# Kernel tuning notes

Hardware: AMD Instinct MI355X
Metric: run time of the kernel (lower is better)

The kernel has to match this reference:

```python
import jax, jax.numpy as jnp
import numpy as np

N_NODES = 100000
N_EDGES = 1000000
D_IN = 64
D_MODEL = 64  # H * D
H = 4
D = D_MODEL // H


def setup_inputs() -> dict:
    key = jax.random.key(0)
    ks = jax.random.split(key, 9)
    nodes = jax.random.normal(ks[0], (N_NODES, D_IN), dtype=jnp.float32)
    senders = jax.random.randint(ks[1], (N_EDGES,), 0, N_NODES, dtype=jnp.int32)
    receivers = jnp.sort(jax.random.randint(ks[2], (N_EDGES,), 0, N_NODES, dtype=jnp.int32))
    s = 1.0 / np.sqrt(D_IN)
    W_qk = jax.random.uniform(ks[3], (D_IN, D_MODEL), jnp.float32, -s, s)
    b_qk = jnp.zeros((D_MODEL,), jnp.float32)
    W_v = jax.random.uniform(ks[4], (D_IN, D_MODEL), jnp.float32, -s, s)
    b_v = jnp.zeros((D_MODEL,), jnp.float32)
    so = 1.0 / np.sqrt(D_MODEL)
    W_out = jax.random.uniform(ks[5], (D_MODEL, D_MODEL), jnp.float32, -so, so)
    b_out = jnp.zeros((D_MODEL,), jnp.float32)
    return {
        'nodes': nodes, 'W_qk': W_qk, 'b_qk': b_qk, 'W_v': W_v, 'b_v': b_v,
        'W_out': W_out, 'b_out': b_out, 'senders': senders, 'receivers': receivers,
    }


def _segment_softmax(logits, segment_ids, num_segments):
    # jraph-style numerically stable segment softmax (segments are sorted)
    maxs = jax.ops.segment_max(logits, segment_ids, num_segments, indices_are_sorted=True)
    e = jnp.exp(logits - maxs[segment_ids])
    z = jax.ops.segment_sum(e, segment_ids, num_segments, indices_are_sorted=True)
    return e / z[segment_ids]


def reference(nodes, W_qk, b_qk, W_v, b_v, W_out, b_out, senders, receivers):
    N = nodes.shape[0]
    # projections: N (H D) -> N H D
    qks = (nodes @ W_qk + b_qk).reshape(N, H, D)
    vs = (nodes @ W_v + b_v).reshape(N, H, D)
    # per-edge QK scores: [E, H]
    scores = jnp.einsum('ehd,ehd->eh', qks[receivers], qks[senders])
    attn = _segment_softmax(scores, receivers, N)
    # weighted message scatter: [E,H,D] -> [N, H*D]
    messages = (attn[..., None] * vs[senders]).reshape(-1, H * D)
    ctx = jax.ops.segment_sum(messages, receivers, N, indices_are_sorted=True)
    out = ctx @ W_out + b_out
    return out, attn
```

## Files before the change

kernel.cpp:

```cpp
#include <hip/hip_runtime.h>
#include <math.h>


typedef _Float16 h2 __attribute__((ext_vector_type(2)));
typedef _Float16 half8 __attribute__((ext_vector_type(8)));
typedef float floatx4 __attribute__((ext_vector_type(4)));

#define SP_ROW 136

__global__ __launch_bounds__(256) void mhga_prep(
    const float* __restrict__ Wqk, const float* __restrict__ Wv,
    _Float16* __restrict__ Wt,
    const int* __restrict__ receivers, int* __restrict__ row_ptr,
    int N, int E)
{
    if ((int)blockIdx.x < 32) {
        const int idx = blockIdx.x * 256 + threadIdx.x;
        const int n = idx >> 6, k = idx & 63;
        const float w = (n < 64) ? Wqk[k * 64 + n] : Wv[k * 64 + (n - 64)];
        Wt[idx] = (_Float16)w;
        return;
    }
    const int n = (blockIdx.x - 32) * 256 + threadIdx.x;
    if (n > N) return;
    int lo = 0, hi = E;
    while (lo < hi) {
        const int mid = (lo + hi) >> 1;
        if (receivers[mid] < n) lo = mid + 1; else hi = mid;
    }
    row_ptr[n] = lo;
}

__global__ __launch_bounds__(256) void mhga_proj(
    const float* __restrict__ X, const _Float16* __restrict__ Wt,
    const float* __restrict__ bqk, const float* __restrict__ bv,
    unsigned char* __restrict__ packed, int N)
{
    __shared__ __align__(16) _Float16 sP[64 * SP_ROW];
    const int t = threadIdx.x;
    const int w = t >> 6, lane = t & 63;
    const int ln = lane & 15, quad = lane >> 4;
    const int m0 = blockIdx.x * 64;

    const int arow = min(m0 + w * 16 + ln, N - 1);
    const float* xr = X + (size_t)arow * 64;
    const float4 xa = *(const float4*)(xr + quad * 8);
    const float4 xb = *(const float4*)(xr + quad * 8 + 4);
    const float4 xc = *(const float4*)(xr + 32 + quad * 8);
    const float4 xd = *(const float4*)(xr + 32 + quad * 8 + 4);
    const half8 a0 = { (_Float16)xa.x, (_Float16)xa.y, (_Float16)xa.z,
                       (_Float16)xa.w, (_Float16)xb.x, (_Float16)xb.y,
                       (_Float16)xb.z, (_Float16)xb.w };
    const half8 a1 = { (_Float16)xc.x, (_Float16)xc.y, (_Float16)xc.z,
                       (_Float16)xc.w, (_Float16)xd.x, (_Float16)xd.y,
                       (_Float16)xd.z, (_Float16)xd.w };

    floatx4 acc[8];
#pragma unroll
    for (int tt = 0; tt < 8; ++tt) {
        const _Float16* wrow = Wt + (tt * 16 + ln) * 64;
        const half8 b0 = *(const half8*)(wrow + quad * 8);
        const half8 b1 = *(const half8*)(wrow + 32 + quad * 8);
        floatx4 c = {0.f, 0.f, 0.f, 0.f};
        c = __builtin_amdgcn_mfma_f32_16x16x32_f16(a0, b0, c, 0, 0, 0);
        c = __builtin_amdgcn_mfma_f32_16x16x32_f16(a1, b1, c, 0, 0, 0);
        acc[tt] = c;
    }

#pragma unroll
    for (int tt = 0; tt < 8; ++tt) {
        const float bt = (tt < 4) ? bqk[tt * 16 + ln] : bv[(tt - 4) * 16 + ln];
        const int j = (tt & 3) * 16 + ln;
        const int fidx = (j >> 2) * 8 + ((tt < 4) ? 0 : 4) + (j & 3);
#pragma unroll
        for (int r = 0; r < 4; ++r) {
            const int lrow = w * 16 + quad * 4 + r;
            sP[lrow * SP_ROW + fidx] = (_Float16)(acc[tt][r] + bt);
        }
    }

    const int crow = w * 16 + (lane >> 2);
    const int grow = m0 + crow;
    if (grow < N) {
        const _Float16* src = sP + crow * SP_ROW + (lane & 3) * 32;
        unsigned char* dst = packed + (size_t)grow * 256 + (lane & 3) * 64;
#pragma unroll
        for (int c = 0; c < 4; ++c)
            *(uint4*)(dst + c * 16) = *(const uint4*)(src + c * 8);
    }
}

__global__ __launch_bounds__(256) void mhga_attn(
    const unsigned char* __restrict__ packed,
    const int* __restrict__ senders, const int* __restrict__ row_ptr,
    const float* __restrict__ Wout, const float* __restrict__ bout,
    float* __restrict__ p_ws, float* __restrict__ out,
    float* __restrict__ attn_out, int N)
{
    __shared__ float sW[64 * 64];
    __shared__ float sCtx[4][64];
    const int t = threadIdx.x;
#pragma unroll
    for (int i = t * 4; i < 4096; i += 1024)
        *(float4*)(sW + i) = *(const float4*)(Wout + i);

    const int wave = t >> 6, lane = t & 63;
    const int g = lane >> 4, tl = lane & 15;
    const float bo = bout[lane];
    __syncthreads();

    for (int n = blockIdx.x * 4 + wave; n < N; n += gridDim.x * 4) {
        const int e0 = row_ptr[n];
        const int e1 = row_ptr[n + 1];
        float l = 0.f;
        float4 ctx = make_float4(0.f, 0.f, 0.f, 0.f);
        const uint4 qpk = *(const uint4*)(packed + (size_t)n * 256 + tl * 16);
        const h2 q0 = __builtin_bit_cast(h2, qpk.x);
        const h2 q1 = __builtin_bit_cast(h2, qpk.y);

        for (int base = e0; base < e1; base += 64) {
            const int cnt = min(64, e1 - base);
            int sid = 0;
            if (base + lane < e1) sid = senders[base + lane];
            const int iters = (cnt + 3) >> 2;
            for (int i = 0; i < iters; ++i) {
                const int idx = i * 4 + g;
                const int s = __shfl(sid, idx, 64);
                if (idx < cnt) {
                    const uint4 pk =
                        *(const uint4*)(packed + (size_t)s * 256 + tl * 16);
                    const h2 k0 = __builtin_bit_cast(h2, pk.x);
                    const h2 k1 = __builtin_bit_cast(h2, pk.y);
                    const h2 v0 = __builtin_bit_cast(h2, pk.z);
                    const h2 v1 = __builtin_bit_cast(h2, pk.w);
                    float d = __builtin_amdgcn_fdot2(q0, k0, 0.f, false);
                    d = __builtin_amdgcn_fdot2(q1, k1, d, false);
                    d += __shfl_xor(d, 1, 64);
                    d += __shfl_xor(d, 2, 64);
                    const float p = __expf(d);
                    if ((tl & 3) == 0)
                        p_ws[(size_t)(base + idx) * 4 + (tl >> 2)] = p;
                    l += p;
                    ctx.x = fmaf(p, (float)v0.x, ctx.x);
                    ctx.y = fmaf(p, (float)v0.y, ctx.y);
                    ctx.z = fmaf(p, (float)v1.x, ctx.z);
                    ctx.w = fmaf(p, (float)v1.y, ctx.w);
                }
            }
        }
#pragma unroll
        for (int mask = 16; mask <= 32; mask <<= 1) {
            l     += __shfl_xor(l, mask, 64);
            ctx.x += __shfl_xor(ctx.x, mask, 64);
            ctx.y += __shfl_xor(ctx.y, mask, 64);
            ctx.z += __shfl_xor(ctx.z, mask, 64);
            ctx.w += __shfl_xor(ctx.w, mask, 64);
        }
        const float inv = (l > 0.f) ? (1.f / l) : 0.f;
        if (g == 0) {
            *(float4*)(&sCtx[wave][tl * 4]) =
                make_float4(ctx.x * inv, ctx.y * inv, ctx.z * inv, ctx.w * inv);
        }

        __builtin_amdgcn_s_waitcnt(0x0F70);

        const float lh = __shfl(l, (lane & 3) << 2, 64);
        const float invl = (lh > 0.f) ? (1.f / lh) : 0.f;
        volatile const float* vp = p_ws;
        for (int f = e0 * 4 + lane; f < e1 * 4; f += 64)
            attn_out[f] = vp[f] * invl;

        float acc = bo;
#pragma unroll
        for (int k = 0; k < 64; k += 4) {
            const float4 c = *(const float4*)(&sCtx[wave][k]);
            acc = fmaf(c.x, sW[(k + 0) * 64 + lane], acc);
            acc = fmaf(c.y, sW[(k + 1) * 64 + lane], acc);
            acc = fmaf(c.z, sW[(k + 2) * 64 + lane], acc);
            acc = fmaf(c.w, sW[(k + 3) * 64 + lane], acc);
        }
        out[(size_t)n * 64 + lane] = acc;
    }
}

extern "C" void kernel_launch(void* const* d_in, const int* in_sizes, int n_in,
                              void* d_out, int out_size, void* d_ws, size_t ws_size,
                              hipStream_t stream) {
    const float* nodes   = (const float*)d_in[0];
    const float* W_qk    = (const float*)d_in[1];
    const float* b_qk    = (const float*)d_in[2];
    const float* W_v     = (const float*)d_in[3];
    const float* b_v     = (const float*)d_in[4];
    const float* W_out   = (const float*)d_in[5];
    const float* b_out   = (const float*)d_in[6];
    const int* senders   = (const int*)d_in[7];
    const int* receivers = (const int*)d_in[8];

    const int N = in_sizes[0] / 64;
    const int E = in_sizes[7];

    float* out      = (float*)d_out;
    float* attn_out = out + (size_t)N * 64;

    unsigned char* packed = (unsigned char*)d_ws;
    int*   rowp = (int*)(packed + (size_t)N * 256);
    float* p_ws = (float*)(rowp + (((N + 1) + 3) & ~3));
    _Float16* Wt = (_Float16*)(p_ws + (size_t)E * 4);

    const int RB = (N + 1 + 255) / 256;
    mhga_prep<<<32 + RB, 256, 0, stream>>>(W_qk, W_v, Wt, receivers, rowp, N, E);
    mhga_proj<<<(N + 63) / 64, 256, 0, stream>>>(nodes, Wt, b_qk, b_v,
                                                 packed, N);
    mhga_attn<<<2048, 256, 0, stream>>>(packed, senders, rowp,
                                        W_out, b_out, p_ws, out, attn_out, N);
}
```

Before: 194.4 us.

## Keep attention probabilities in registers and process eight edges per wave step

The attention kernel now maps each edge to 8 lanes that load 32 bytes each, instead of 16 lanes loading 16 bytes, so each wave step covers eight edges. For receivers with at most 64 edges the unnormalized probabilities stay in registers and are normalized directly into attn_out, which removes the p_ws scratch write, the readback, and the waitcnt. Receivers with more edges take a fallback that recomputes the scores in a second pass. The cost is more registers for ctx[8] and preg[8], plus redundant gathers on high-degree nodes.

```diff
diff --git a/kernel.cpp b/kernel.cpp
--- a/kernel.cpp
+++ b/kernel.cpp
@@ -94,8 +94,7 @@
     const unsigned char* __restrict__ packed,
     const int* __restrict__ senders, const int* __restrict__ row_ptr,
     const float* __restrict__ Wout, const float* __restrict__ bout,
-    float* __restrict__ p_ws, float* __restrict__ out,
-    float* __restrict__ attn_out, int N)
+    float* __restrict__ out, float* __restrict__ attn_out, int N)
 {
     __shared__ float sW[64 * 64];
     __shared__ float sCtx[4][64];
@@ -105,70 +104,149 @@
         *(float4*)(sW + i) = *(const float4*)(Wout + i);
 
     const int wave = t >> 6, lane = t & 63;
-    const int g = lane >> 4, tl = lane & 15;
+    const int g = lane >> 3, u = lane & 7;
     const float bo = bout[lane];
     __syncthreads();
 
     for (int n = blockIdx.x * 4 + wave; n < N; n += gridDim.x * 4) {
         const int e0 = row_ptr[n];
         const int e1 = row_ptr[n + 1];
+        const int cnt = e1 - e0;
+
+        const unsigned char* qrow = packed + (size_t)n * 256 + u * 32;
+        const uint4 qA = *(const uint4*)(qrow);
+        const uint4 qB = *(const uint4*)(qrow + 16);
+        const h2 q0 = __builtin_bit_cast(h2, qA.x);
+        const h2 q1 = __builtin_bit_cast(h2, qA.y);
+        const h2 q2 = __builtin_bit_cast(h2, qB.x);
+        const h2 q3 = __builtin_bit_cast(h2, qB.y);
+
         float l = 0.f;
-        float4 ctx = make_float4(0.f, 0.f, 0.f, 0.f);
-        const uint4 qpk = *(const uint4*)(packed + (size_t)n * 256 + tl * 16);
-        const h2 q0 = __builtin_bit_cast(h2, qpk.x);
-        const h2 q1 = __builtin_bit_cast(h2, qpk.y);
-
-        for (int base = e0; base < e1; base += 64) {
-            const int cnt = min(64, e1 - base);
+        float ctx[8] = {0.f, 0.f, 0.f, 0.f, 0.f, 0.f, 0.f, 0.f};
+        float preg[8];
+        int iters = 0;
+
+        if (cnt <= 64) {
             int sid = 0;
-            if (base + lane < e1) sid = senders[base + lane];
-            const int iters = (cnt + 3) >> 2;
-            for (int i = 0; i < iters; ++i) {
-                const int idx = i * 4 + g;
+            if (e0 + lane < e1) sid = senders[e0 + lane];
+            iters = (cnt + 7) >> 3;
+#pragma unroll
+            for (int i = 0; i < 8; ++i) {
+                if (i >= iters) break;
+                const int idx = i * 8 + g;
                 const int s = __shfl(sid, idx, 64);
-                if (idx < cnt) {
-                    const uint4 pk =
-                        *(const uint4*)(packed + (size_t)s * 256 + tl * 16);
-                    const h2 k0 = __builtin_bit_cast(h2, pk.x);
-                    const h2 k1 = __builtin_bit_cast(h2, pk.y);
-                    const h2 v0 = __builtin_bit_cast(h2, pk.z);
-                    const h2 v1 = __builtin_bit_cast(h2, pk.w);
-                    float d = __builtin_amdgcn_fdot2(q0, k0, 0.f, false);
-                    d = __builtin_amdgcn_fdot2(q1, k1, d, false);
+                const unsigned char* row = packed + (size_t)s * 256 + u * 32;
+                const uint4 A = *(const uint4*)(row);
+                const uint4 B = *(const uint4*)(row + 16);
+                float d = __builtin_amdgcn_fdot2(q0, __builtin_bit_cast(h2, A.x), 0.f, false);
+                d = __builtin_amdgcn_fdot2(q1, __builtin_bit_cast(h2, A.y), d, false);
+                d = __builtin_amdgcn_fdot2(q2, __builtin_bit_cast(h2, B.x), d, false);
+                d = __builtin_amdgcn_fdot2(q3, __builtin_bit_cast(h2, B.y), d, false);
+                d += __shfl_xor(d, 1, 64);
+                float p = __expf(d);
+                p = (idx < cnt) ? p : 0.f;
+                preg[i] = p;
+                l += p;
+                const h2 vA0 = __builtin_bit_cast(h2, A.z);
+                const h2 vA1 = __builtin_bit_cast(h2, A.w);
+                const h2 vB0 = __builtin_bit_cast(h2, B.z);
+                const h2 vB1 = __builtin_bit_cast(h2, B.w);
+                ctx[0] = fmaf(p, (float)vA0.x, ctx[0]);
+                ctx[1] = fmaf(p, (float)vA0.y, ctx[1]);
+                ctx[2] = fmaf(p, (float)vA1.x, ctx[2]);
+                ctx[3] = fmaf(p, (float)vA1.y, ctx[3]);
+                ctx[4] = fmaf(p, (float)vB0.x, ctx[4]);
+                ctx[5] = fmaf(p, (float)vB0.y, ctx[5]);
+                ctx[6] = fmaf(p, (float)vB1.x, ctx[6]);
+                ctx[7] = fmaf(p, (float)vB1.y, ctx[7]);
+            }
+        } else {
+            for (int base = e0; base < e1; base += 64) {
+                const int c2 = min(64, e1 - base);
+                int sid = 0;
+                if (base + lane < e1) sid = senders[base + lane];
+                const int it2 = (c2 + 7) >> 3;
+                for (int i = 0; i < it2; ++i) {
+                    const int idx = i * 8 + g;
+                    const int s = __shfl(sid, idx, 64);
+                    const unsigned char* row = packed + (size_t)s * 256 + u * 32;
+                    const uint4 A = *(const uint4*)(row);
+                    const uint4 B = *(const uint4*)(row + 16);
+                    float d = __builtin_amdgcn_fdot2(q0, __builtin_bit_cast(h2, A.x), 0.f, false);
+                    d = __builtin_amdgcn_fdot2(q1, __builtin_bit_cast(h2, A.y), d, false);
+                    d = __builtin_amdgcn_fdot2(q2, __builtin_bit_cast(h2, B.x), d, false);
+                    d = __builtin_amdgcn_fdot2(q3, __builtin_bit_cast(h2, B.y), d, false);
                     d += __shfl_xor(d, 1, 64);
-                    d += __shfl_xor(d, 2, 64);
-                    const float p = __expf(d);
-                    if ((tl & 3) == 0)
-                        p_ws[(size_t)(base + idx) * 4 + (tl >> 2)] = p;
+                    float p = __expf(d);
+                    p = (idx < c2) ? p : 0.f;
                     l += p;
-                    ctx.x = fmaf(p, (float)v0.x, ctx.x);
-                    ctx.y = fmaf(p, (float)v0.y, ctx.y);
-                    ctx.z = fmaf(p, (float)v1.x, ctx.z);
-                    ctx.w = fmaf(p, (float)v1.y, ctx.w);
+                    const h2 vA0 = __builtin_bit_cast(h2, A.z);
+                    const h2 vA1 = __builtin_bit_cast(h2, A.w);
+                    const h2 vB0 = __builtin_bit_cast(h2, B.z);
+                    const h2 vB1 = __builtin_bit_cast(h2, B.w);
+                    ctx[0] = fmaf(p, (float)vA0.x, ctx[0]);
+                    ctx[1] = fmaf(p, (float)vA0.y, ctx[1]);
+                    ctx[2] = fmaf(p, (float)vA1.x, ctx[2]);
+                    ctx[3] = fmaf(p, (float)vA1.y, ctx[3]);
+                    ctx[4] = fmaf(p, (float)vB0.x, ctx[4]);
+                    ctx[5] = fmaf(p, (float)vB0.y, ctx[5]);
+                    ctx[6] = fmaf(p, (float)vB1.x, ctx[6]);
+                    ctx[7] = fmaf(p, (float)vB1.y, ctx[7]);
                 }
             }
         }
-#pragma unroll
-        for (int mask = 16; mask <= 32; mask <<= 1) {
-            l     += __shfl_xor(l, mask, 64);
-            ctx.x += __shfl_xor(ctx.x, mask, 64);
-            ctx.y += __shfl_xor(ctx.y, mask, 64);
-            ctx.z += __shfl_xor(ctx.z, mask, 64);
-            ctx.w += __shfl_xor(ctx.w, mask, 64);
+
+#pragma unroll
+        for (int mask = 8; mask <= 32; mask <<= 1) {
+            l += __shfl_xor(l, mask, 64);
+#pragma unroll
+            for (int j = 0; j < 8; ++j)
+                ctx[j] += __shfl_xor(ctx[j], mask, 64);
         }
         const float inv = (l > 0.f) ? (1.f / l) : 0.f;
+
+        if (cnt <= 64) {
+            if ((u & 1) == 0) {
+                const int h = u >> 1;
+#pragma unroll
+                for (int i = 0; i < 8; ++i) {
+                    const int idx = i * 8 + g;
+                    if (i < iters && idx < cnt)
+                        attn_out[(size_t)(e0 + idx) * 4 + h] = preg[i] * inv;
+                }
+            }
+        } else {
+            for (int base = e0; base < e1; base += 64) {
+                const int c2 = min(64, e1 - base);
+                int sid = 0;
+                if (base + lane < e1) sid = senders[base + lane];
+                const int it2 = (c2 + 7) >> 3;
+                for (int i = 0; i < it2; ++i) {
+                    const int idx = i * 8 + g;
+                    const int s = __shfl(sid, idx, 64);
+                    if (idx < c2) {
+                        const unsigned char* row = packed + (size_t)s * 256 + u * 32;
+                        const uint4 A = *(const uint4*)(row);
+                        const uint4 B = *(const uint4*)(row + 16);
+                        float d = __builtin_amdgcn_fdot2(q0, __builtin_bit_cast(h2, A.x), 0.f, false);
+                        d = __builtin_amdgcn_fdot2(q1, __builtin_bit_cast(h2, A.y), d, false);
+                        d = __builtin_amdgcn_fdot2(q2, __builtin_bit_cast(h2, B.x), d, false);
+                        d = __builtin_amdgcn_fdot2(q3, __builtin_bit_cast(h2, B.y), d, false);
+                        d += __shfl_xor(d, 1, 64);
+                        const float p = __expf(d);
+                        if ((u & 1) == 0)
+                            attn_out[(size_t)(base + idx) * 4 + (u >> 1)] = p * inv;
+                    }
+                }
+            }
+        }
+
         if (g == 0) {
-            *(float4*)(&sCtx[wave][tl * 4]) =
-                make_float4(ctx.x * inv, ctx.y * inv, ctx.z * inv, ctx.w * inv);
-        }
-
-        __builtin_amdgcn_s_waitcnt(0x0F70);
-
-        const float lh = __shfl(l, (lane & 3) << 2, 64);
-        const float invl = (lh > 0.f) ? (1.f / lh) : 0.f;
-        volatile const float* vp = p_ws;
-        for (int f = e0 * 4 + lane; f < e1 * 4; f += 64)
-            attn_out[f] = vp[f] * invl;
+            *(float4*)(&sCtx[wave][u * 8]) =
+                make_float4(ctx[0] * inv, ctx[1] * inv, ctx[2] * inv, ctx[3] * inv);
+            *(float4*)(&sCtx[wave][u * 8 + 4]) =
+                make_float4(ctx[4] * inv, ctx[5] * inv, ctx[6] * inv, ctx[7] * inv);
+        }
 
         float acc = bo;
 #pragma unroll
@@ -212,5 +290,5 @@
     mhga_proj<<<(N + 63) / 64, 256, 0, stream>>>(nodes, Wt, b_qk, b_v,
                                                  packed, N);
     mhga_attn<<<2048, 256, 0, stream>>>(packed, senders, rowp,
-                                        W_out, b_out, p_ws, out, attn_out, N);
-}
+                                        W_out, b_out, out, attn_out, N);
+}
```

Result: slower. 214.2 us (+10.2%).

## Process two receiver nodes per wave and stage attention weights in LDS

Applied to the files above, without the earlier changes.

Each wave now handles a pair of consecutive receiver nodes, loading both nodes' sender IDs in one 64-lane read and interleaving their gathers so more loads are in flight at once. When the pair has at most 64 edges, unnormalised attention weights are kept in shared memory rather than written to and re-read from a global scratch buffer. Pairs with more edges take a fallback path that writes raw weights into the output buffer and rescales them in place. The output projection is computed for both nodes in one pass over the W_out tile held in shared memory, and launch bounds request higher occupancy. In exchange the code has more branching and higher register pressure.

```diff
diff --git a/kernel.cpp b/kernel.cpp
--- a/kernel.cpp
+++ b/kernel.cpp
@@ -90,15 +90,14 @@
     }
 }
 
-__global__ __launch_bounds__(256) void mhga_attn(
+__global__ __launch_bounds__(256, 8) void mhga_attn(
     const unsigned char* __restrict__ packed,
     const int* __restrict__ senders, const int* __restrict__ row_ptr,
     const float* __restrict__ Wout, const float* __restrict__ bout,
-    float* __restrict__ p_ws, float* __restrict__ out,
-    float* __restrict__ attn_out, int N)
+    float* __restrict__ out, float* __restrict__ attn_out, int N)
 {
     __shared__ float sW[64 * 64];
-    __shared__ float sCtx[4][64];
+    __shared__ float sAtt[4][256];
     const int t = threadIdx.x;
 #pragma unroll
     for (int i = t * 4; i < 4096; i += 1024)
@@ -109,77 +108,194 @@
     const float bo = bout[lane];
     __syncthreads();
 
-    for (int n = blockIdx.x * 4 + wave; n < N; n += gridDim.x * 4) {
-        const int e0 = row_ptr[n];
-        const int e1 = row_ptr[n + 1];
-        float l = 0.f;
-        float4 ctx = make_float4(0.f, 0.f, 0.f, 0.f);
-        const uint4 qpk = *(const uint4*)(packed + (size_t)n * 256 + tl * 16);
-        const h2 q0 = __builtin_bit_cast(h2, qpk.x);
-        const h2 q1 = __builtin_bit_cast(h2, qpk.y);
-
-        for (int base = e0; base < e1; base += 64) {
-            const int cnt = min(64, e1 - base);
+    const int P = (N + 1) >> 1;
+    for (int pr = blockIdx.x * 4 + wave; pr < P; pr += gridDim.x * 4) {
+        const int n0 = pr * 2, n1 = n0 + 1;
+        const int e0 = row_ptr[n0];
+        const int e1 = row_ptr[n1];
+        const int e2 = (n1 < N) ? row_ptr[n1 + 1] : e1;
+        const int cnt0 = e1 - e0, cnt1 = e2 - e1, cntT = e2 - e0;
+
+        const uint4 q0pk = *(const uint4*)(packed + (size_t)n0 * 256 + tl * 16);
+        const int n1c = min(n1, N - 1);
+        const uint4 q1pk = *(const uint4*)(packed + (size_t)n1c * 256 + tl * 16);
+        const h2 qa0 = __builtin_bit_cast(h2, q0pk.x);
+        const h2 qa1 = __builtin_bit_cast(h2, q0pk.y);
+        const h2 qb0 = __builtin_bit_cast(h2, q1pk.x);
+        const h2 qb1 = __builtin_bit_cast(h2, q1pk.y);
+
+        float l0 = 0.f, l1 = 0.f;
+        float4 c0 = make_float4(0.f, 0.f, 0.f, 0.f);
+        float4 c1 = make_float4(0.f, 0.f, 0.f, 0.f);
+        const bool slow = (cntT > 64);
+
+        if (!slow) {
             int sid = 0;
-            if (base + lane < e1) sid = senders[base + lane];
-            const int iters = (cnt + 3) >> 2;
-            for (int i = 0; i < iters; ++i) {
+            if (e0 + lane < e2) sid = senders[e0 + lane];
+            const int it0 = (cnt0 + 3) >> 2;
+            const int it1 = (cnt1 + 3) >> 2;
+            const int im = max(it0, it1);
+            for (int i = 0; i < im; ++i) {
                 const int idx = i * 4 + g;
-                const int s = __shfl(sid, idx, 64);
-                if (idx < cnt) {
-                    const uint4 pk =
-                        *(const uint4*)(packed + (size_t)s * 256 + tl * 16);
-                    const h2 k0 = __builtin_bit_cast(h2, pk.x);
-                    const h2 k1 = __builtin_bit_cast(h2, pk.y);
-                    const h2 v0 = __builtin_bit_cast(h2, pk.z);
-                    const h2 v1 = __builtin_bit_cast(h2, pk.w);
-                    float d = __builtin_amdgcn_fdot2(q0, k0, 0.f, false);
-                    d = __builtin_amdgcn_fdot2(q1, k1, d, false);
+                const bool doA = (i < it0), doB = (i < it1);
+                uint4 pkA, pkB;
+                if (doA) {
+                    const int sA = __shfl(sid, idx, 64);
+                    pkA = *(const uint4*)(packed + (size_t)sA * 256 + tl * 16);
+                }
+                if (doB) {
+                    const int sB = __shfl(sid, (cnt0 + idx) & 63, 64);
+                    pkB = *(const uint4*)(packed + (size_t)sB * 256 + tl * 16);
+                }
+                if (doA) {
+                    const h2 k0 = __builtin_bit_cast(h2, pkA.x);
+                    const h2 k1 = __builtin_bit_cast(h2, pkA.y);
+                    const h2 v0 = __builtin_bit_cast(h2, pkA.z);
+                    const h2 v1 = __builtin_bit_cast(h2, pkA.w);
+                    float d = __builtin_amdgcn_fdot2(qa0, k0, 0.f, false);
+                    d = __builtin_amdgcn_fdot2(qa1, k1, d, false);
                     d += __shfl_xor(d, 1, 64);
                     d += __shfl_xor(d, 2, 64);
-                    const float p = __expf(d);
-                    if ((tl & 3) == 0)
-                        p_ws[(size_t)(base + idx) * 4 + (tl >> 2)] = p;
-                    l += p;
-                    ctx.x = fmaf(p, (float)v0.x, ctx.x);
-                    ctx.y = fmaf(p, (float)v0.y, ctx.y);
-                    ctx.z = fmaf(p, (float)v1.x, ctx.z);
-                    ctx.w = fmaf(p, (float)v1.y, ctx.w);
+                    float p = __expf(d);
+                    p = (idx < cnt0) ? p : 0.f;
+                    if ((tl & 3) == 0 && idx < cnt0)
+                        sAtt[wave][idx * 4 + (tl >> 2)] = p;
+                    l0 += p;
+                    c0.x = fmaf(p, (float)v0.x, c0.x);
+                    c0.y = fmaf(p, (float)v0.y, c0.y);
+                    c0.z = fmaf(p, (float)v1.x, c0.z);
+                    c0.w = fmaf(p, (float)v1.y, c0.w);
+                }
+                if (doB) {
+                    const h2 k0 = __builtin_bit_cast(h2, pkB.x);
+                    const h2 k1 = __builtin_bit_cast(h2, pkB.y);
+                    const h2 v0 = __builtin_bit_cast(h2, pkB.z);
+                    const h2 v1 = __builtin_bit_cast(h2, pkB.w);
+                    float d = __builtin_amdgcn_fdot2(qb0, k0, 0.f, false);
+                    d = __builtin_amdgcn_fdot2(qb1, k1, d, false);
+                    d += __shfl_xor(d, 1, 64);
+                    d += __shfl_xor(d, 2, 64);
+                    float p = __expf(d);
+                    p = (idx < cnt1) ? p : 0.f;
+                    if ((tl & 3) == 0 && idx < cnt1)
+                        sAtt[wave][(cnt0 + idx) * 4 + (tl >> 2)] = p;
+                    l1 += p;
+                    c1.x = fmaf(p, (float)v0.x, c1.x);
+                    c1.y = fmaf(p, (float)v0.y, c1.y);
+                    c1.z = fmaf(p, (float)v1.x, c1.z);
+                    c1.w = fmaf(p, (float)v1.y, c1.w);
                 }
             }
-        }
+        } else {
+            for (int m = 0; m < 2; ++m) {
+                const int s0 = m ? e1 : e0, s1 = m ? e2 : e1;
+                const h2 qq0 = m ? qb0 : qa0, qq1 = m ? qb1 : qa1;
+                for (int base = s0; base < s1; base += 64) {
+                    const int c2 = min(64, s1 - base);
+                    int sid2 = 0;
+                    if (base + lane < s1) sid2 = senders[base + lane];
+                    const int it2 = (c2 + 3) >> 2;
+                    for (int i = 0; i < it2; ++i) {
+                        const int idx = i * 4 + g;
+                        const int s = __shfl(sid2, idx, 64);
+                        if (idx < c2) {
+                            const uint4 pk =
+                                *(const uint4*)(packed + (size_t)s * 256 + tl * 16);
+                            const h2 k0 = __builtin_bit_cast(h2, pk.x);
+                            const h2 k1 = __builtin_bit_cast(h2, pk.y);
+                            const h2 v0 = __builtin_bit_cast(h2, pk.z);
+                            const h2 v1 = __builtin_bit_cast(h2, pk.w);
+                            float d = __builtin_amdgcn_fdot2(qq0, k0, 0.f, false);
+                            d = __builtin_amdgcn_fdot2(qq1, k1, d, false);
+                            d += __shfl_xor(d, 1, 64);
+                            d += __shfl_xor(d, 2, 64);
+                            const float p = __expf(d);
+                            if ((tl & 3) == 0)
+                                attn_out[(size_t)(base + idx) * 4 + (tl >> 2)] = p;
+                            if (m == 0) {
+                                l0 += p;
+                                c0.x = fmaf(p, (float)v0.x, c0.x);
+                                c0.y = fmaf(p, (float)v0.y, c0.y);
+                                c0.z = fmaf(p, (float)v1.x, c0.z);
+                                c0.w = fmaf(p, (float)v1.y, c0.w);
+                            } else {
+                                l1 += p;
+                                c1.x = fmaf(p, (float)v0.x, c1.x);
+                                c1.y = fmaf(p, (float)v0.y, c1.y);
+                                c1.z = fmaf(p, (float)v1.x, c1.z);
+                                c1.w = fmaf(p, (float)v1.y, c1.w);
+                            }
+                        }
+                    }
+                }
+            }
+        }
+
 #pragma unroll
         for (int mask = 16; mask <= 32; mask <<= 1) {
-            l     += __shfl_xor(l, mask, 64);
-            ctx.x += __shfl_xor(ctx.x, mask, 64);
-            ctx.y += __shfl_xor(ctx.y, mask, 64);
-            ctx.z += __shfl_xor(ctx.z, mask, 64);
-            ctx.w += __shfl_xor(ctx.w, mask, 64);
-        }
-        const float inv = (l > 0.f) ? (1.f / l) : 0.f;
+            l0   += __shfl_xor(l0, mask, 64);
+            l1   += __shfl_xor(l1, mask, 64);
+            c0.x += __shfl_xor(c0.x, mask, 64);
+            c0.y += __shfl_xor(c0.y, mask, 64);
+            c0.z += __shfl_xor(c0.z, mask, 64);
+            c0.w += __shfl_xor(c0.w, mask, 64);
+            c1.x += __shfl_xor(c1.x, mask, 64);
+            c1.y += __shfl_xor(c1.y, mask, 64);
+            c1.z += __shfl_xor(c1.z, mask, 64);
+            c1.w += __shfl_xor(c1.w, mask, 64);
+        }
+        const float inv0 = (l0 > 0.f) ? (1.f / l0) : 0.f;
+        const float inv1 = (l1 > 0.f) ? (1.f / l1) : 0.f;
+
+        const float lh0 = __shfl(l0, (lane & 3) << 2, 64);
+        const float lh1 = __shfl(l1, (lane & 3) << 2, 64);
+        const float iv0 = (lh0 > 0.f) ? (1.f / lh0) : 0.f;
+        const float iv1 = (lh1 > 0.f) ? (1.f / lh1) : 0.f;
+        if (!slow) {
+            const int fT = cntT * 4, f0 = cnt0 * 4;
+            for (int f = lane; f < fT; f += 64) {
+                const float iv = (f < f0) ? iv0 : iv1;
+                attn_out[e0 * 4 + f] = sAtt[wave][f] * iv;
+            }
+        } else {
+            __builtin_amdgcn_s_waitcnt(0x0F70);
+            volatile const float* vp = attn_out;
+            for (int f = e0 * 4 + lane; f < e2 * 4; f += 64) {
+                const float iv = (f < e1 * 4) ? iv0 : iv1;
+                attn_out[f] = vp[f] * iv;
+            }
+        }
+
         if (g == 0) {
-            *(float4*)(&sCtx[wave][tl * 4]) =
-                make_float4(ctx.x * inv, ctx.y * inv, ctx.z * inv, ctx.w * inv);
-        }
-
-        __builtin_amdgcn_s_waitcnt(0x0F70);
-
-        const float lh = __shfl(l, (lane & 3) << 2, 64);
-        const float invl = (lh > 0.f) ? (1.f / lh) : 0.f;
-        volatile const float* vp = p_ws;
-        for (int f = e0 * 4 + lane; f < e1 * 4; f += 64)
-            attn_out[f] = vp[f] * invl;
-
-        float acc = bo;
-#pragma unroll
-        for (int k = 0; k < 64; k += 4) {
-            const float4 c = *(const float4*)(&sCtx[wave][k]);
-            acc = fmaf(c.x, sW[(k + 0) * 64 + lane], acc);
-            acc = fmaf(c.y, sW[(k + 1) * 64 + lane], acc);
-            acc = fmaf(c.z, sW[(k + 2) * 64 + lane], acc);
-            acc = fmaf(c.w, sW[(k + 3) * 64 + lane], acc);
-        }
-        out[(size_t)n * 64 + lane] = acc;
+            *(float4*)(&sAtt[wave][tl * 4]) =
+                make_float4(c0.x * inv0, c0.y * inv0, c0.z * inv0, c0.w * inv0);
+        } else if (g == 1) {
+            *(float4*)(&sAtt[wave][64 + tl * 4]) =
+                make_float4(c1.x * inv1, c1.y * inv1, c1.z * inv1, c1.w * inv1);
+        }
+
+        const float* sC0 = &sAtt[wave][0];
+        const float* sC1 = &sAtt[wave][64];
+        float a0 = bo, a1 = 0.f, b0 = bo, b1 = 0.f;
+#pragma unroll
+        for (int k = 0; k < 64; k += 8) {
+            const float4 x0 = *(const float4*)(sC0 + k);
+            const float4 x1 = *(const float4*)(sC0 + k + 4);
+            const float4 y0 = *(const float4*)(sC1 + k);
+            const float4 y1 = *(const float4*)(sC1 + k + 4);
+            float w;
+            w = sW[(k + 0) * 64 + lane]; a0 = fmaf(x0.x, w, a0); b0 = fmaf(y0.x, w, b0);
+            w = sW[(k + 1) * 64 + lane]; a0 = fmaf(x0.y, w, a0); b0 = fmaf(y0.y, w, b0);
+            w = sW[(k + 2) * 64 + lane]; a0 = fmaf(x0.z, w, a0); b0 = fmaf(y0.z, w, b0);
+            w = sW[(k + 3) * 64 + lane]; a0 = fmaf(x0.w, w, a0); b0 = fmaf(y0.w, w, b0);
+            w = sW[(k + 4) * 64 + lane]; a1 = fmaf(x1.x, w, a1); b1 = fmaf(y1.x, w, b1);
+            w = sW[(k + 5) * 64 + lane]; a1 = fmaf(x1.y, w, a1); b1 = fmaf(y1.y, w, b1);
+            w = sW[(k + 6) * 64 + lane]; a1 = fmaf(x1.z, w, a1); b1 = fmaf(y1.z, w, b1);
+            w = sW[(k + 7) * 64 + lane]; a1 = fmaf(x1.w, w, a1); b1 = fmaf(y1.w, w, b1);
+        }
+        out[(size_t)n0 * 64 + lane] = a0 + a1;
+        if (n1 < N)
+            out[(size_t)n1 * 64 + lane] = b0 + b1;
     }
 }
 
@@ -204,13 +320,13 @@
 
     unsigned char* packed = (unsigned char*)d_ws;
     int*   rowp = (int*)(packed + (size_t)N * 256);
-    float* p_ws = (float*)(rowp + (((N + 1) + 3) & ~3));
-    _Float16* Wt = (_Float16*)(p_ws + (size_t)E * 4);
+    float* spare = (float*)(rowp + (((N + 1) + 3) & ~3));
+    _Float16* Wt = (_Float16*)(spare + (size_t)E * 4);
 
     const int RB = (N + 1 + 255) / 256;
     mhga_prep<<<32 + RB, 256, 0, stream>>>(W_qk, W_v, Wt, receivers, rowp, N, E);
     mhga_proj<<<(N + 63) / 64, 256, 0, stream>>>(nodes, Wt, b_qk, b_v,
                                                  packed, N);
     mhga_attn<<<2048, 256, 0, stream>>>(packed, senders, rowp,
-                                        W_out, b_out, p_ws, out, attn_out, N);
+                                        W_out, b_out, out, attn_out, N);
 }
```

Result: slower. 426.6 us (+119.5%).
